# Kernel optimization log

Measured on AMD Instinct MI355X. Metric: run time of the kernel, lower is better.

## Reference

```python
import jax, jax.numpy as jnp
import numpy as np

G = 64        # proteins per batch (groups in structure.indices)
L = 4096      # residues per protein
S = 65536     # sampled pairs per protein (self.samples)
N = G * L     # total residues
P = G * S     # total pairs


def setup_inputs() -> dict:
    key = jax.random.key(0)
    k_in, k_tg, k_l, k_o = jax.random.split(key, 4)
    inputs = jax.random.normal(k_in, (N, 3, 3), dtype=jnp.float32)
    target = jax.random.normal(k_tg, (N, 3, 3), dtype=jnp.float32)
    mask = jnp.ones((N,), dtype=jnp.float32)
    # per-group random pair sampling (torch.randint(total, total+count, (S,2)) per group),
    # with left != right so the distance is never exactly 0 (keeps norm grad finite)
    left_local = jax.random.randint(k_l, (G, S), 0, L)
    offset = jax.random.randint(k_o, (G, S), 1, L)
    right_local = (left_local + offset) % L
    base = (jnp.arange(G, dtype=jnp.int64) * L)[:, None]
    left = (base + left_local).reshape(-1).astype(jnp.int64)
    right = (base + right_local).reshape(-1).astype(jnp.int64)
    return {"inputs": inputs, "target": target, "mask": mask,
            "left": left, "right": right}


def reference(inputs, target, mask, left, right):
    # mask is all-ones -> the (mask > 0) row filtering is the identity.
    ca_in = inputs[:, 1]   # [N, 3] CA coordinates
    ca_tg = target[:, 1]   # [N, 3]
    in_distance = jnp.linalg.norm(ca_in[left] - ca_in[right], axis=1)      # [P]
    target_distance = jnp.linalg.norm(ca_tg[left] - ca_tg[right], axis=1)  # [P]
    result = in_distance - target_distance
    # relative=False -> no denominator rescale
    return jnp.mean(result ** 2)
```

## Files before the change

### kernel.cpp

```cpp
#include <hip/hip_runtime.h>
#include <math.h>

#define Gg 64
#define Ll 4096
#define Ss 65536
#define Nn (Gg * Ll)
#define PAIR_BLOCK 1024
#define CHUNKS 8
#define PAIR_BLOCKS (Gg * CHUNKS)
#define PAIRS_PER_BLOCK (Ss / CHUNKS)
#define ITERS (PAIRS_PER_BLOCK / PAIR_BLOCK)

#define K_CHUNKS 32
#define DIR_BLOCKS (Gg * K_CHUNKS)
#define DIR_PAIRS (Ss / K_CHUNKS)
#define BLOCK 256

typedef _Float16 h2 __attribute__((ext_vector_type(2)));
typedef _Float16 h8 __attribute__((ext_vector_type(8)));

__device__ inline float dot2f16(h2 a, h2 b, float c) {
#if __has_builtin(__builtin_amdgcn_fdot2)
  return __builtin_amdgcn_fdot2(a, b, c, false);
#else
  return fmaf((float)a[0], (float)b[0], fmaf((float)a[1], (float)b[1], c));
#endif
}

__global__ __launch_bounds__(BLOCK) void compact16_kernel(
    const float* __restrict__ inp, const float* __restrict__ tgt,
    h8* __restrict__ comb) {
  int i = blockIdx.x * BLOCK + threadIdx.x;
  if (i >= Nn) return;
  const float* a = inp + (size_t)i * 9 + 3;
  const float* b = tgt + (size_t)i * 9 + 3;
  h8 row;
  row[0] = (_Float16)a[0];
  row[1] = (_Float16)a[1];
  row[2] = (_Float16)b[0];
  row[3] = (_Float16)b[1];
  row[4] = (_Float16)a[2];
  row[5] = (_Float16)b[2];
  row[6] = (_Float16)0.f;
  row[7] = (_Float16)0.f;
  comb[i] = row;
}

template <typename IT>
__global__ __launch_bounds__(PAIR_BLOCK) void pair16_kernel(
    const h8* __restrict__ comb,
    const IT* __restrict__ left, const IT* __restrict__ right,
    float* __restrict__ partial) {
  __shared__ h8 tile[Ll];

  int bid = blockIdx.x;
  int xcd = bid & 7;
  int j = bid >> 3;
  int gi = j & 7;
  int chunk = j >> 3;
  int group = xcd * 8 + gi;

  const h8* src = comb + (size_t)group * Ll;
  for (int k = threadIdx.x; k < Ll; k += PAIR_BLOCK) tile[k] = src[k];
  __syncthreads();

  size_t base = (size_t)group * Ss + (size_t)chunk * PAIRS_PER_BLOCK;
  float acc = 0.f;
#pragma unroll
  for (int t = 0; t < ITERS; ++t) {
    size_t p = base + (size_t)t * PAIR_BLOCK + threadIdx.x;
    int li = (int)left[p] & (Ll - 1);
    int ri = (int)right[p] & (Ll - 1);
    h8 L = tile[li];
    h8 R = tile[ri];
    h8 D = L - R;
    h2 d01 = __builtin_shufflevector(D, D, 0, 1);
    h2 d23 = __builtin_shufflevector(D, D, 2, 3);
    float dzi = (float)D[4];
    float dzt = (float)D[5];
    float din2 = dot2f16(d01, d01, dzi * dzi);
    float dtg2 = dot2f16(d23, d23, dzt * dzt);
    float d = sqrtf(din2) - sqrtf(dtg2);
    acc = fmaf(d, d, acc);
  }

  for (int off = 32; off; off >>= 1) acc += __shfl_down(acc, off, 64);
  __shared__ float wsum[PAIR_BLOCK / 64];
  if ((threadIdx.x & 63) == 0) wsum[threadIdx.x >> 6] = acc;
  __syncthreads();
  if (threadIdx.x == 0) {
    float s = 0.f;
    for (int w = 0; w < PAIR_BLOCK / 64; ++w) s += wsum[w];
    partial[bid] = s;
  }
}

template <typename IT>
__global__ __launch_bounds__(BLOCK) void pair_kernel_direct(
    const float* __restrict__ inp, const float* __restrict__ tgt,
    const IT* __restrict__ left, const IT* __restrict__ right,
    float* __restrict__ partial) {
  int bid = blockIdx.x;
  int x = bid & 7;
  int j = bid >> 3;
  int group = x + 8 * (j / K_CHUNKS);
  int chunk = j % K_CHUNKS;
  size_t base = (size_t)group * Ss + (size_t)chunk * DIR_PAIRS;

  float acc = 0.f;
  for (int t = threadIdx.x; t < DIR_PAIRS; t += BLOCK) {
    size_t p = base + t;
    size_t li = (size_t)left[p] * 9 + 3;
    size_t ri = (size_t)right[p] * 9 + 3;
    float dx = inp[li + 0] - inp[ri + 0];
    float dy = inp[li + 1] - inp[ri + 1];
    float dz = inp[li + 2] - inp[ri + 2];
    float tx = tgt[li + 0] - tgt[ri + 0];
    float ty = tgt[li + 1] - tgt[ri + 1];
    float tz = tgt[li + 2] - tgt[ri + 2];
    float din = sqrtf(dx * dx + dy * dy + dz * dz);
    float dtg = sqrtf(tx * tx + ty * ty + tz * tz);
    float d = din - dtg;
    acc += d * d;
  }

  for (int off = 32; off; off >>= 1) acc += __shfl_down(acc, off, 64);
  __shared__ float wsum[BLOCK / 64];
  if ((threadIdx.x & 63) == 0) wsum[threadIdx.x >> 6] = acc;
  __syncthreads();
  if (threadIdx.x == 0) {
    float s = 0.f;
    for (int w = 0; w < BLOCK / 64; ++w) s += wsum[w];
    partial[bid] = s;
  }
}

__global__ __launch_bounds__(BLOCK) void reduce_kernel(
    const float* __restrict__ partial, int n, float* __restrict__ out) {
  double acc = 0.0;
  for (int i = threadIdx.x; i < n; i += BLOCK)
    acc += (double)partial[i];
  for (int off = 32; off; off >>= 1) acc += __shfl_down(acc, off, 64);
  __shared__ double wsum[BLOCK / 64];
  if ((threadIdx.x & 63) == 0) wsum[threadIdx.x >> 6] = acc;
  __syncthreads();
  if (threadIdx.x == 0) {
    double s = 0.0;
    for (int w = 0; w < BLOCK / 64; ++w) s += wsum[w];
    out[0] = (float)(s / (double)((size_t)Gg * Ss));
  }
}

extern "C" void kernel_launch(void* const* d_in, const int* in_sizes, int n_in,
                              void* d_out, int out_size, void* d_ws, size_t ws_size,
                              hipStream_t stream) {
  const float* inp = (const float*)d_in[0];
  const float* tgt = (const float*)d_in[1];
  const void* leftp = d_in[3];
  const void* rightp = d_in[4];
  float* out = (float*)d_out;

  const int P = Gg * Ss;
  const bool idx64 = (in_sizes[3] == 2 * P);

  size_t combBytes = (size_t)Nn * sizeof(h8);
  size_t partBytes = (size_t)DIR_BLOCKS * sizeof(float);

  if (ws_size >= combBytes + partBytes) {
    h8* comb = (h8*)d_ws;
    float* partial = (float*)((char*)d_ws + combBytes);
    compact16_kernel<<<Nn / BLOCK, BLOCK, 0, stream>>>(inp, tgt, comb);
    if (idx64) {
      pair16_kernel<long long><<<PAIR_BLOCKS, PAIR_BLOCK, 0, stream>>>(
          comb, (const long long*)leftp, (const long long*)rightp, partial);
    } else {
      pair16_kernel<int><<<PAIR_BLOCKS, PAIR_BLOCK, 0, stream>>>(
          comb, (const int*)leftp, (const int*)rightp, partial);
    }
    reduce_kernel<<<1, BLOCK, 0, stream>>>(partial, PAIR_BLOCKS, out);
  } else {
    float* partial = (float*)d_ws;
    if (idx64) {
      pair_kernel_direct<long long><<<DIR_BLOCKS, BLOCK, 0, stream>>>(
          inp, tgt, (const long long*)leftp, (const long long*)rightp, partial);
    } else {
      pair_kernel_direct<int><<<DIR_BLOCKS, BLOCK, 0, stream>>>(
          inp, tgt, (const int*)leftp, (const int*)rightp, partial);
    }
    reduce_kernel<<<1, BLOCK, 0, stream>>>(partial, DIR_BLOCKS, out);
  }
}
```

Before: 21.94 us.

## Fuse final reduction into pair kernel via fixed-point atomics and vectorize index loads

For 32-bit indices, the pair kernel now accumulates block sums into a fixed-point 64-bit atomic counter. The last block to finish writes the mean directly, which removes the separate reduce kernel launch. The LDS tile is filled with global_load_lds direct-to-LDS loads, and left/right indices are read as int2 pairs. This adds atomic contention and fixed-point rounding in exchange for one fewer launch and wider loads; the accumulator is zeroed inside the compaction kernel.

```diff
diff --git a/kernel.cpp b/kernel.cpp
--- a/kernel.cpp
+++ b/kernel.cpp
@@ -9,12 +9,12 @@
 #define CHUNKS 8
 #define PAIR_BLOCKS (Gg * CHUNKS)
 #define PAIRS_PER_BLOCK (Ss / CHUNKS)
-#define ITERS (PAIRS_PER_BLOCK / PAIR_BLOCK)
+#define BLOCK 256
+#define SCALE 1048576.0
 
 #define K_CHUNKS 32
 #define DIR_BLOCKS (Gg * K_CHUNKS)
 #define DIR_PAIRS (Ss / K_CHUNKS)
-#define BLOCK 256
 
 typedef _Float16 h2 __attribute__((ext_vector_type(2)));
 typedef _Float16 h8 __attribute__((ext_vector_type(8)));
@@ -29,7 +29,11 @@
 
 __global__ __launch_bounds__(BLOCK) void compact16_kernel(
     const float* __restrict__ inp, const float* __restrict__ tgt,
-    h8* __restrict__ comb) {
+    h8* __restrict__ comb, unsigned long long* __restrict__ acc) {
+  if (blockIdx.x == 0 && threadIdx.x == 0) {
+    acc[0] = 0ull;
+    acc[1] = 0ull;
+  }
   int i = blockIdx.x * BLOCK + threadIdx.x;
   if (i >= Nn) return;
   const float* a = inp + (size_t)i * 9 + 3;
@@ -46,11 +50,10 @@
   comb[i] = row;
 }
 
-template <typename IT>
-__global__ __launch_bounds__(PAIR_BLOCK) void pair16_kernel(
+__global__ __launch_bounds__(PAIR_BLOCK) void pair16v_kernel(
     const h8* __restrict__ comb,
-    const IT* __restrict__ left, const IT* __restrict__ right,
-    float* __restrict__ partial) {
+    const int* __restrict__ left, const int* __restrict__ right,
+    unsigned long long* __restrict__ acc, float* __restrict__ out) {
   __shared__ h8 tile[Ll];
 
   int bid = blockIdx.x;
@@ -60,15 +63,96 @@
   int chunk = j >> 3;
   int group = xcd * 8 + gi;
 
+  int tid = threadIdx.x;
+  int wave = tid >> 6;
+  int lane = tid & 63;
+
+  const char* gs = (const char*)(comb + (size_t)group * Ll);
+  char* ls = (char*)tile;
+#if __has_builtin(__builtin_amdgcn_global_load_lds)
+  typedef __attribute__((address_space(1))) const void gv_t;
+  typedef __attribute__((address_space(3))) void lv_t;
+#pragma unroll
+  for (int k = 0; k < 4; ++k) {
+    int c = wave * 4 + k;
+    __builtin_amdgcn_global_load_lds(
+        (gv_t*)(gs + (size_t)c * 1024 + (size_t)lane * 16),
+        (lv_t*)(ls + (size_t)c * 1024), 16, 0, 0);
+  }
+  asm volatile("s_waitcnt vmcnt(0)" ::: "memory");
+#else
+  {
+    const h8* src = (const h8*)gs;
+    for (int k = tid; k < Ll; k += PAIR_BLOCK) tile[k] = src[k];
+  }
+#endif
+  __syncthreads();
+
+  size_t base = (size_t)group * Ss + (size_t)chunk * PAIRS_PER_BLOCK;
+  const int2* lp = (const int2*)(left + base);
+  const int2* rp = (const int2*)(right + base);
+
+  float facc = 0.f;
+#pragma unroll
+  for (int k = 0; k < 4; ++k) {
+    int2 L2 = lp[k * PAIR_BLOCK + tid];
+    int2 R2 = rp[k * PAIR_BLOCK + tid];
+#pragma unroll
+    for (int s = 0; s < 2; ++s) {
+      int li = (s ? L2.y : L2.x) & (Ll - 1);
+      int ri = (s ? R2.y : R2.x) & (Ll - 1);
+      h8 L = tile[li];
+      h8 R = tile[ri];
+      h8 D = L - R;
+      h2 d01 = __builtin_shufflevector(D, D, 0, 1);
+      h2 d23 = __builtin_shufflevector(D, D, 2, 3);
+      float dzi = (float)D[4];
+      float dzt = (float)D[5];
+      float din2 = dot2f16(d01, d01, dzi * dzi);
+      float dtg2 = dot2f16(d23, d23, dzt * dzt);
+      float d = sqrtf(din2) - sqrtf(dtg2);
+      facc = fmaf(d, d, facc);
+    }
+  }
+
+  for (int off = 32; off; off >>= 1) facc += __shfl_down(facc, off, 64);
+  __shared__ float wsum[PAIR_BLOCK / 64];
+  if (lane == 0) wsum[wave] = facc;
+  __syncthreads();
+  if (tid == 0) {
+    double s = 0.0;
+    for (int w = 0; w < PAIR_BLOCK / 64; ++w) s += (double)wsum[w];
+    long long q = llrint(s * SCALE);
+    atomicAdd(&acc[0], (unsigned long long)q);
+    __threadfence();
+    unsigned int t = (unsigned int)atomicAdd(&acc[1], 1ull);
+    if (t == (unsigned int)gridDim.x - 1) {
+      unsigned long long tot = atomicAdd(&acc[0], 0ull);
+      out[0] = (float)((double)(long long)tot / SCALE /
+                       (double)((size_t)Gg * Ss));
+    }
+  }
+}
+
+__global__ __launch_bounds__(PAIR_BLOCK) void pair16_i64_kernel(
+    const h8* __restrict__ comb,
+    const long long* __restrict__ left, const long long* __restrict__ right,
+    float* __restrict__ partial) {
+  __shared__ h8 tile[Ll];
+  int bid = blockIdx.x;
+  int xcd = bid & 7;
+  int j = bid >> 3;
+  int group = xcd * 8 + (j & 7);
+  int chunk = j >> 3;
+
   const h8* src = comb + (size_t)group * Ll;
   for (int k = threadIdx.x; k < Ll; k += PAIR_BLOCK) tile[k] = src[k];
   __syncthreads();
 
   size_t base = (size_t)group * Ss + (size_t)chunk * PAIRS_PER_BLOCK;
   float acc = 0.f;
-#pragma unroll
-  for (int t = 0; t < ITERS; ++t) {
-    size_t p = base + (size_t)t * PAIR_BLOCK + threadIdx.x;
+  for (int t = threadIdx.x; t < PAIRS_PER_BLOCK; t += PAIR_BLOCK) {
+    size_t p = base + t;
     int li = (int)left[p] & (Ll - 1);
     int ri = (int)right[p] & (Ll - 1);
     h8 L = tile[li];
@@ -83,7 +167,6 @@
     float d = sqrtf(din2) - sqrtf(dtg2);
     acc = fmaf(d, d, acc);
   }
-
   for (int off = 32; off; off >>= 1) acc += __shfl_down(acc, off, 64);
   __shared__ float wsum[PAIR_BLOCK / 64];
   if ((threadIdx.x & 63) == 0) wsum[threadIdx.x >> 6] = acc;
@@ -123,7 +206,6 @@
     float d = din - dtg;
     acc += d * d;
   }
-
   for (int off = 32; off; off >>= 1) acc += __shfl_down(acc, off, 64);
   __shared__ float wsum[BLOCK / 64];
   if ((threadIdx.x & 63) == 0) wsum[threadIdx.x >> 6] = acc;
@@ -138,8 +220,7 @@
 __global__ __launch_bounds__(BLOCK) void reduce_kernel(
     const float* __restrict__ partial, int n, float* __restrict__ out) {
   double acc = 0.0;
-  for (int i = threadIdx.x; i < n; i += BLOCK)
-    acc += (double)partial[i];
+  for (int i = threadIdx.x; i < n; i += BLOCK) acc += (double)partial[i];
   for (int off = 32; off; off >>= 1) acc += __shfl_down(acc, off, 64);
   __shared__ double wsum[BLOCK / 64];
   if ((threadIdx.x & 63) == 0) wsum[threadIdx.x >> 6] = acc;
@@ -164,20 +245,24 @@
   const bool idx64 = (in_sizes[3] == 2 * P);
 
   size_t combBytes = (size_t)Nn * sizeof(h8);
+  size_t accBytes = 2 * sizeof(unsigned long long);
   size_t partBytes = (size_t)DIR_BLOCKS * sizeof(float);
 
-  if (ws_size >= combBytes + partBytes) {
+  if (ws_size >= combBytes + accBytes + partBytes) {
     h8* comb = (h8*)d_ws;
-    float* partial = (float*)((char*)d_ws + combBytes);
-    compact16_kernel<<<Nn / BLOCK, BLOCK, 0, stream>>>(inp, tgt, comb);
+    unsigned long long* acc =
+        (unsigned long long*)((char*)d_ws + combBytes);
+    float* partial = (float*)((char*)d_ws + combBytes + accBytes);
+
+    compact16_kernel<<<Nn / BLOCK, BLOCK, 0, stream>>>(inp, tgt, comb, acc);
     if (idx64) {
-      pair16_kernel<long long><<<PAIR_BLOCKS, PAIR_BLOCK, 0, stream>>>(
+      pair16_i64_kernel<<<PAIR_BLOCKS, PAIR_BLOCK, 0, stream>>>(
           comb, (const long long*)leftp, (const long long*)rightp, partial);
+      reduce_kernel<<<1, BLOCK, 0, stream>>>(partial, PAIR_BLOCKS, out);
     } else {
-      pair16_kernel<int><<<PAIR_BLOCKS, PAIR_BLOCK, 0, stream>>>(
-          comb, (const int*)leftp, (const int*)rightp, partial);
-    }
-    reduce_kernel<<<1, BLOCK, 0, stream>>>(partial, PAIR_BLOCKS, out);
+      pair16v_kernel<<<PAIR_BLOCKS, PAIR_BLOCK, 0, stream>>>(
+          comb, (const int*)leftp, (const int*)rightp, acc, out);
+    }
   } else {
     float* partial = (float*)d_ws;
     if (idx64) {
```

After: 32.09 us. +46.3%, slower.

## Fuse fp16 compaction into pair kernel and vectorize int32 index loads

Applied to the files above, without the earlier changes.

Drops the separate compaction kernel and its global round trip. Each pair block now builds the fp16 CA tile for its group in LDS straight from the input and target arrays. Index loads become int4 vector loads, with the first batch issued before the tile build to overlap latency. The cost is that every block re-reads and re-converts its group's coordinates (8 chunks per group, so 8x redundant reads), and the fast path only covers int32 indices; 64-bit indices fall back to the slower direct kernel.

```diff
diff --git a/kernel.cpp b/kernel.cpp
--- a/kernel.cpp
+++ b/kernel.cpp
@@ -5,19 +5,20 @@
 #define Ll 4096
 #define Ss 65536
 #define Nn (Gg * Ll)
-#define PAIR_BLOCK 1024
+#define PB 1024
 #define CHUNKS 8
 #define PAIR_BLOCKS (Gg * CHUNKS)
-#define PAIRS_PER_BLOCK (Ss / CHUNKS)
-#define ITERS (PAIRS_PER_BLOCK / PAIR_BLOCK)
+#define PPB (Ss / CHUNKS)
+#define BLOCK 256
 
 #define K_CHUNKS 32
 #define DIR_BLOCKS (Gg * K_CHUNKS)
 #define DIR_PAIRS (Ss / K_CHUNKS)
-#define BLOCK 256
 
 typedef _Float16 h2 __attribute__((ext_vector_type(2)));
 typedef _Float16 h8 __attribute__((ext_vector_type(8)));
+
+struct f3 { float x, y, z; };
 
 __device__ inline float dot2f16(h2 a, h2 b, float c) {
 #if __has_builtin(__builtin_amdgcn_fdot2)
@@ -27,70 +28,81 @@
 #endif
 }
 
-__global__ __launch_bounds__(BLOCK) void compact16_kernel(
+#define PAIR_STEP(LI, RI)                                        \
+  do {                                                           \
+    h8 Lv = tile[(LI) & (Ll - 1)];                               \
+    h8 Rv = tile[(RI) & (Ll - 1)];                               \
+    h8 Dv = Lv - Rv;                                             \
+    h2 d01 = __builtin_shufflevector(Dv, Dv, 0, 1);              \
+    h2 d23 = __builtin_shufflevector(Dv, Dv, 2, 3);              \
+    float dzi = (float)Dv[4];                                    \
+    float dzt = (float)Dv[5];                                    \
+    float din2 = dot2f16(d01, d01, dzi * dzi);                   \
+    float dtg2 = dot2f16(d23, d23, dzt * dzt);                   \
+    float dd = sqrtf(din2) - sqrtf(dtg2);                        \
+    facc = fmaf(dd, dd, facc);                                   \
+  } while (0)
+
+__global__ __launch_bounds__(PB) void fused_kernel(
     const float* __restrict__ inp, const float* __restrict__ tgt,
-    h8* __restrict__ comb) {
-  int i = blockIdx.x * BLOCK + threadIdx.x;
-  if (i >= Nn) return;
-  const float* a = inp + (size_t)i * 9 + 3;
-  const float* b = tgt + (size_t)i * 9 + 3;
-  h8 row;
-  row[0] = (_Float16)a[0];
-  row[1] = (_Float16)a[1];
-  row[2] = (_Float16)b[0];
-  row[3] = (_Float16)b[1];
-  row[4] = (_Float16)a[2];
-  row[5] = (_Float16)b[2];
-  row[6] = (_Float16)0.f;
-  row[7] = (_Float16)0.f;
-  comb[i] = row;
-}
-
-template <typename IT>
-__global__ __launch_bounds__(PAIR_BLOCK) void pair16_kernel(
-    const h8* __restrict__ comb,
-    const IT* __restrict__ left, const IT* __restrict__ right,
+    const int* __restrict__ left, const int* __restrict__ right,
     float* __restrict__ partial) {
   __shared__ h8 tile[Ll];
 
   int bid = blockIdx.x;
   int xcd = bid & 7;
   int j = bid >> 3;
-  int gi = j & 7;
+  int group = xcd * 8 + (j & 7);
   int chunk = j >> 3;
-  int group = xcd * 8 + gi;
+  int tid = threadIdx.x;
 
-  const h8* src = comb + (size_t)group * Ll;
-  for (int k = threadIdx.x; k < Ll; k += PAIR_BLOCK) tile[k] = src[k];
+  size_t base = (size_t)group * Ss + (size_t)chunk * PPB;
+  const int4* lp = (const int4*)(left + base);
+  const int4* rp = (const int4*)(right + base);
+  int4 L0 = lp[tid];
+  int4 R0 = rp[tid];
+
+  const float* ib = inp + (size_t)group * Ll * 9 + 3;
+  const float* tb = tgt + (size_t)group * Ll * 9 + 3;
+#pragma unroll
+  for (int q = 0; q < 4; ++q) {
+    int row = q * PB + tid;
+    f3 a = *(const f3*)(ib + (size_t)row * 9);
+    f3 b = *(const f3*)(tb + (size_t)row * 9);
+    h8 r;
+    r[0] = (_Float16)a.x;
+    r[1] = (_Float16)a.y;
+    r[2] = (_Float16)b.x;
+    r[3] = (_Float16)b.y;
+    r[4] = (_Float16)a.z;
+    r[5] = (_Float16)b.z;
+    r[6] = (_Float16)0.f;
+    r[7] = (_Float16)0.f;
+    tile[row] = r;
+  }
   __syncthreads();
 
-  size_t base = (size_t)group * Ss + (size_t)chunk * PAIRS_PER_BLOCK;
-  float acc = 0.f;
-#pragma unroll
-  for (int t = 0; t < ITERS; ++t) {
-    size_t p = base + (size_t)t * PAIR_BLOCK + threadIdx.x;
-    int li = (int)left[p] & (Ll - 1);
-    int ri = (int)right[p] & (Ll - 1);
-    h8 L = tile[li];
-    h8 R = tile[ri];
-    h8 D = L - R;
-    h2 d01 = __builtin_shufflevector(D, D, 0, 1);
-    h2 d23 = __builtin_shufflevector(D, D, 2, 3);
-    float dzi = (float)D[4];
-    float dzt = (float)D[5];
-    float din2 = dot2f16(d01, d01, dzi * dzi);
-    float dtg2 = dot2f16(d23, d23, dzt * dzt);
-    float d = sqrtf(din2) - sqrtf(dtg2);
-    acc = fmaf(d, d, acc);
-  }
+  float facc = 0.f;
+  int4 L1 = lp[PB + tid];
+  int4 R1 = rp[PB + tid];
+  PAIR_STEP(L0.x, R0.x);
+  PAIR_STEP(L0.y, R0.y);
+  PAIR_STEP(L0.z, R0.z);
+  PAIR_STEP(L0.w, R0.w);
+  PAIR_STEP(L1.x, R1.x);
+  PAIR_STEP(L1.y, R1.y);
+  PAIR_STEP(L1.z, R1.z);
+  PAIR_STEP(L1.w, R1.w);
 
-  for (int off = 32; off; off >>= 1) acc += __shfl_down(acc, off, 64);
-  __shared__ float wsum[PAIR_BLOCK / 64];
-  if ((threadIdx.x & 63) == 0) wsum[threadIdx.x >> 6] = acc;
+  for (int off = 32; off; off >>= 1) facc += __shfl_down(facc, off, 64);
+  __shared__ float wsum[PB / 64];
+  int lane = tid & 63;
+  int wave = tid >> 6;
+  if (lane == 0) wsum[wave] = facc;
   __syncthreads();
-  if (threadIdx.x == 0) {
+  if (tid == 0) {
     float s = 0.f;
-    for (int w = 0; w < PAIR_BLOCK / 64; ++w) s += wsum[w];
+    for (int w = 0; w < PB / 64; ++w) s += wsum[w];
     partial[bid] = s;
   }
 }
@@ -123,7 +135,6 @@
     float d = din - dtg;
     acc += d * d;
   }
-
   for (int off = 32; off; off >>= 1) acc += __shfl_down(acc, off, 64);
   __shared__ float wsum[BLOCK / 64];
   if ((threadIdx.x & 63) == 0) wsum[threadIdx.x >> 6] = acc;
@@ -138,8 +149,7 @@
 __global__ __launch_bounds__(BLOCK) void reduce_kernel(
     const float* __restrict__ partial, int n, float* __restrict__ out) {
   double acc = 0.0;
-  for (int i = threadIdx.x; i < n; i += BLOCK)
-    acc += (double)partial[i];
+  for (int i = threadIdx.x; i < n; i += BLOCK) acc += (double)partial[i];
   for (int off = 32; off; off >>= 1) acc += __shfl_down(acc, off, 64);
   __shared__ double wsum[BLOCK / 64];
   if ((threadIdx.x & 63) == 0) wsum[threadIdx.x >> 6] = acc;
@@ -163,20 +173,12 @@
   const int P = Gg * Ss;
   const bool idx64 = (in_sizes[3] == 2 * P);
 
-  size_t combBytes = (size_t)Nn * sizeof(h8);
   size_t partBytes = (size_t)DIR_BLOCKS * sizeof(float);
 
-  if (ws_size >= combBytes + partBytes) {
-    h8* comb = (h8*)d_ws;
-    float* partial = (float*)((char*)d_ws + combBytes);
-    compact16_kernel<<<Nn / BLOCK, BLOCK, 0, stream>>>(inp, tgt, comb);
-    if (idx64) {
-      pair16_kernel<long long><<<PAIR_BLOCKS, PAIR_BLOCK, 0, stream>>>(
-          comb, (const long long*)leftp, (const long long*)rightp, partial);
-    } else {
-      pair16_kernel<int><<<PAIR_BLOCKS, PAIR_BLOCK, 0, stream>>>(
-          comb, (const int*)leftp, (const int*)rightp, partial);
-    }
+  if (!idx64 && ws_size >= partBytes) {
+    float* partial = (float*)d_ws;
+    fused_kernel<<<PAIR_BLOCKS, PB, 0, stream>>>(
+        inp, tgt, (const int*)leftp, (const int*)rightp, partial);
     reduce_kernel<<<1, BLOCK, 0, stream>>>(partial, PAIR_BLOCKS, out);
   } else {
     float* partial = (float*)d_ws;
```

Result: faster. 19.69 us (-10.3%).
